# Optimization experiments

Measured on AMD Instinct MI355X. Metric: run time of the kernel, lower is better.

## Reference

```python
import jax, jax.numpy as jnp
import numpy as np

B, H = 8, 8
C_IN, C_OUT = 128, 128
E, O = C_IN // H, C_OUT // H              # per-head channels
S = (32, 32, 64)                           # spatial dims (space_dims_q == space_dims_kv)
M = (8, 8, 8)                              # lowest-mode block kept per rfft dim
N_MODES = M[0] * M[1] * M[2]               # 512 = mask.sum()
SCALE = 1.0 / (C_IN * C_OUT)


def setup_inputs() -> dict:
    key = jax.random.key(0)
    k1, k2, k3, k4 = jax.random.split(key, 4)
    q = jax.random.normal(k1, (B, H, E) + S, dtype=jnp.float32)
    k = jax.random.normal(k2, (B, H, E) + S, dtype=jnp.float32)
    # torch.rand(..., dtype=cfloat): real and imag parts each uniform [0,1), scaled
    w_re = jax.random.uniform(k3, (H, E, O, N_MODES), dtype=jnp.float32) * SCALE
    w_im = jax.random.uniform(k4, (H, E, O, N_MODES), dtype=jnp.float32) * SCALE
    return {"q": q, "k": k, "w_re": w_re, "w_im": w_im}


def _select_modes(x_ft):
    # block low-mode mask -> slice + flatten (C order, matches torch bool indexing)
    m0, m1, m2 = M
    return x_ft[..., :m0, :m1, :m2].reshape(x_ft.shape[:3] + (-1,))


def reference(q, k, w_re, w_im):
    m0, m1, m2 = M
    xq_ft = jnp.fft.rfftn(q, axes=(3, 4, 5), norm='ortho')   # [B,H,E,32,32,33] c64
    xk_ft = jnp.fft.rfftn(k, axes=(3, 4, 5), norm='ortho')
    xq_sel = _select_modes(xq_ft)                             # [B,H,E,Mq]
    xk_sel = _select_modes(xk_ft)                             # [B,H,E,Mkv]
    w = jax.lax.complex(w_re, w_im)                           # [H,E,O,Mq]

    # complex attention: no conjugation, complex tanh (matches torch)
    att = jnp.tanh(jnp.einsum('bhex,bhey->bhxy', xq_sel, xk_sel))
    xqkv = jnp.einsum('bhxy,bhey->bhex', att, xk_sel)         # [B,H,E,Mq]
    xqkvw = jnp.einsum('bhex,heox->bhox', xqkv, w)            # [B,H,O,Mq]

    out_ft = jnp.zeros((q.shape[0], H, O, S[0], S[1], S[2] // 2 + 1),
                       dtype=xqkvw.dtype)
    out_ft = out_ft.at[..., :m0, :m1, :m2].set(
        xqkvw.reshape(q.shape[0], H, O, m0, m1, m2))

    # canonical_fft_freq over dims (3,4): x <- (x + conj(x[-i mod s0, -j mod s1]))/2
    neg = jnp.roll(jnp.flip(out_ft, axis=(3, 4)), shift=(1, 1), axis=(3, 4))
    out_ft = (out_ft + jnp.conj(neg)) * 0.5

    out = jnp.fft.irfftn(out_ft / (C_IN * C_OUT), axes=(3, 4, 5), s=S, norm='ortho')
    return out  # original returns (out, None)
```

## Files before the change

### kernel.cpp

```cpp
#include <hip/hip_runtime.h>

#define PI_F 3.14159265358979323846f

template<int v> struct ic_t { static constexpr int value = v; };

template<int N, int I = 0, typename F>
__device__ __forceinline__ void sfor(F&& f) {
  if constexpr (I < N) { f(ic_t<I>{}); sfor<N, I + 1>(static_cast<F&&>(f)); }
}

__host__ __device__ constexpr int fold_idx(int t) {
  t &= 63;
  return (t <= 16) ? t : (t <= 32) ? (32 - t) : (t <= 48) ? (t - 32) : (64 - t);
}
__host__ __device__ constexpr float fold_sgn(int t) {
  t &= 63;
  return (t <= 16) ? 1.f : (t <= 48) ? -1.f : 1.f;
}

__device__ constexpr float CCV[17] = {
  1.0f, 0.9951847266721969f, 0.9807852804032304f, 0.9569403357322088f,
  0.9238795325112867f, 0.8819212643483550f, 0.8314696123025452f,
  0.7730104533627370f, 0.7071067811865476f, 0.6343932841636455f,
  0.5555702330196022f, 0.4713967368259976f, 0.3826834323650898f,
  0.2902846772544623f, 0.1950903220161283f, 0.0980171403295606f, 0.0f};

#define TCOS(T) (fold_sgn(T) * CCV[fold_idx(T)])
#define TSIN(T) (fold_sgn(((T) + 48) & 63) * CCV[fold_idx(((T) + 48) & 63)])

template<int G>
__device__ __forceinline__ void row_group(const float4& qa, const float4& qb,
                                          const float4& qc, const float4& qd,
                                          float* Xr, float* Xi)
{
  sfor<4>([&](auto MC) {
    constexpr int m = decltype(MC)::value;
    constexpr int j = 4 * G + m;
    const float xa = (m == 0) ? qa.x : (m == 1) ? qa.y : (m == 2) ? qa.z : qa.w;
    const float xb = (m == 0) ? qb.x : (m == 1) ? qb.y : (m == 2) ? qb.z : qb.w;
    const float xc = (m == 0) ? qc.x : (m == 1) ? qc.y : (m == 2) ? qc.z : qc.w;
    const float xd = (m == 0) ? qd.x : (m == 1) ? qd.y : (m == 2) ? qd.z : qd.w;
    const float s02 = xa + xc, d02 = xa - xc;
    const float s13 = xb + xd, d31 = xd - xb;
    const float g0 = s02 + s13, g2 = s02 - s13;
    Xr[0] += g0;
    sfor<3>([&](auto EC) {
      constexpr int k2 = 2 * (decltype(EC)::value + 1);
      constexpr int t = (k2 * j) & 63;
      const float g = (k2 == 4) ? g0 : g2;
      Xr[k2] = fmaf(g,  TCOS(t), Xr[k2]);
      Xi[k2] = fmaf(-g, TSIN(t), Xi[k2]);
    });
    sfor<4>([&](auto UC) {
      constexpr int k2 = 2 * decltype(UC)::value + 1;
      constexpr int t = (k2 * j) & 63;
      const float gr = d02;
      const float gi = ((k2 & 3) == 1) ? d31 : -d31;
      Xr[k2] = fmaf(gr, TCOS(t), fmaf(gi,  TSIN(t), Xr[k2]));
      Xi[k2] = fmaf(gi, TCOS(t), fmaf(-gr, TSIN(t), Xi[k2]));
    });
  });
}

__global__ __launch_bounds__(512, 4)
void k1_fwd_dft(const float* __restrict__ qg, const float* __restrict__ kg,
                float2* __restrict__ qsel, float2* __restrict__ ksel)
{
  __shared__ float2 Yb[8 * 1036];
  __shared__ float2 tw32[32];

  const int tid = threadIdx.x;
  const int lane = tid & 63;
  const int wv = tid >> 6;
  const int bid = blockIdx.x;
  const int ch = bid & 1023;
  const float* __restrict__ src = (bid < 1024 ? qg : kg) + (size_t)ch * 65536;
  float2* __restrict__ dst = (bid < 1024 ? qsel : ksel) + ch * 512;

  if (tid < 32) {
    float s, c;
    sincosf((float)tid * (2.f * PI_F / 32.f), &s, &c);
    tw32[tid] = make_float2(c, s);
  }

  #pragma unroll
  for (int p = 0; p < 2; ++p) {
    const int row = (p << 9) + tid;
    const float4* __restrict__ rq = (const float4*)(src + ((size_t)row << 6));
    float Xr[8], Xi[8];
    sfor<8>([&](auto K) { constexpr int k = decltype(K)::value;
      Xr[k] = 0.f; Xi[k] = 0.f; });

    float4 A0 = rq[0], A1 = rq[4], A2 = rq[8],  A3 = rq[12];
    float4 B0 = rq[1], B1 = rq[5], B2 = rq[9],  B3 = rq[13];
    __builtin_amdgcn_sched_barrier(0);
    row_group<0>(A0, A1, A2, A3, Xr, Xi);
    __builtin_amdgcn_sched_barrier(0);
    A0 = rq[2]; A1 = rq[6]; A2 = rq[10]; A3 = rq[14];
    __builtin_amdgcn_sched_barrier(0);
    row_group<1>(B0, B1, B2, B3, Xr, Xi);
    __builtin_amdgcn_sched_barrier(0);
    B0 = rq[3]; B1 = rq[7]; B2 = rq[11]; B3 = rq[15];
    __builtin_amdgcn_sched_barrier(0);
    row_group<2>(A0, A1, A2, A3, Xr, Xi);
    __builtin_amdgcn_sched_barrier(0);
    row_group<3>(B0, B1, B2, B3, Xr, Xi);

    sfor<8>([&](auto KC) {
      constexpr int k2 = decltype(KC)::value;
      Yb[k2 * 1036 + row] = make_float2(Xr[k2], Xi[k2]);
    });
  }
  __syncthreads();

  const int k1 = lane >> 3;
  const int k2 = lane & 7;
  float Wr[8], Wi[8];
  sfor<8>([&](auto K) { constexpr int k = decltype(K)::value;
    Wr[k] = 0.f; Wi[k] = 0.f; });

  sfor<4>([&](auto QC) {
    constexpr int q = decltype(QC)::value;
    const int n0 = wv + 8 * q;
    const float2* __restrict__ yp = &Yb[k2 * 1036 + n0 * 32];
    float zr = 0.f, zi = 0.f;
    #pragma unroll
    for (int n1 = 0; n1 < 32; ++n1) {
      const float2 y = yp[n1];
      const float2 w = tw32[(k1 * n1) & 31];
      zr = fmaf(y.x, w.x, fmaf( y.y, w.y, zr));
      zi = fmaf(y.y, w.x, fmaf(-y.x, w.y, zi));
    }
    sfor<8>([&](auto KC) {
      constexpr int k0 = decltype(KC)::value;
      const float2 w = tw32[(k0 * n0) & 31];
      Wr[k0] = fmaf(zr, w.x, fmaf( zi, w.y, Wr[k0]));
      Wi[k0] = fmaf(zi, w.x, fmaf(-zr, w.y, Wi[k0]));
    });
  });
  __syncthreads();

  float2* __restrict__ part = Yb;
  sfor<8>([&](auto KC) {
    constexpr int k0 = decltype(KC)::value;
    part[k0 * 512 + (wv << 6) + lane] = make_float2(Wr[k0], Wi[k0]);
  });
  __syncthreads();

  {
    const float2* __restrict__ pp = &part[(wv << 9) + lane];
    float sr = 0.f, si = 0.f;
    #pragma unroll
    for (int w8 = 0; w8 < 8; ++w8) {
      const float2 v = pp[w8 * 64];
      sr += v.x; si += v.y;
    }
    dst[tid] = make_float2(sr * (1.f / 256.f), si * (1.f / 256.f));
  }
}

__global__ __launch_bounds__(512, 4)
void k2_attn(const float2* __restrict__ qsel, const float2* __restrict__ ksel,
             float2* __restrict__ xqkv)
{
  __shared__ float2 Kl[8192];
  const int tid = threadIdx.x;
  const int bh = blockIdx.x >> 3;
  const int xo = blockIdx.x & 7;

  const float2* __restrict__ kb = ksel + bh * 8192;
  for (int i = tid; i < 8192; i += 512) Kl[i] = kb[i];

  const int xr = tid & 63;
  const int yh = tid >> 6;
  const int x = xo * 64 + xr;
  const float2* __restrict__ qb = qsel + bh * 8192;
  float qr[16], qi[16], ar[16], ai[16];
  sfor<16>([&](auto E) {
    constexpr int e = decltype(E)::value;
    const float2 v = qb[e * 512 + x];
    qr[e] = v.x; qi[e] = v.y;
    ar[e] = 0.f; ai[e] = 0.f;
  });
  __syncthreads();

  const int y0 = yh * 64;
  for (int y = y0; y < y0 + 64; ++y) {
    float kr[16], ki[16];
    float sr = 0.f, si = 0.f;
    sfor<16>([&](auto E) {
      constexpr int e = decltype(E)::value;
      const float2 v = Kl[e * 512 + y];
      kr[e] = v.x; ki[e] = v.y;
      sr = fmaf(qr[e], v.x, fmaf(-qi[e], v.y, sr));
      si = fmaf(qr[e], v.y, fmaf( qi[e], v.x, si));
    });
    float a2 = 2.f * sr;
    a2 = fminf(fmaxf(a2, -30.f), 30.f);
    const float b2 = 2.f * si;
    const float ea = expf(a2);
    const float ei = 1.f / ea;
    const float sh = 0.5f * (ea - ei);
    const float chp = 0.5f * (ea + ei);
    float sb, cb;
    sincosf(b2, &sb, &cb);
    const float inv = 1.f / (chp + cb);
    const float tr = sh * inv;
    const float ti = sb * inv;
    sfor<16>([&](auto E) {
      constexpr int e = decltype(E)::value;
      ar[e] = fmaf(tr, kr[e], fmaf(-ti, ki[e], ar[e]));
      ai[e] = fmaf(tr, ki[e], fmaf( ti, kr[e], ai[e]));
    });
  }
  __syncthreads();
  float* __restrict__ red = (float*)Kl;
  if (yh) {
    const int g = yh - 1;
    sfor<16>([&](auto E) {
      constexpr int e = decltype(E)::value;
      red[(g * 32 + 2 * e) * 64 + xr] = ar[e];
      red[(g * 32 + 2 * e + 1) * 64 + xr] = ai[e];
    });
  }
  __syncthreads();
  if (!yh) {
    float2* __restrict__ ob = xqkv + bh * 8192;
    sfor<16>([&](auto E) {
      constexpr int e = decltype(E)::value;
      float sr2 = ar[e], si2 = ai[e];
      #pragma unroll
      for (int g = 0; g < 7; ++g) {
        sr2 += red[(g * 32 + 2 * e) * 64 + xr];
        si2 += red[(g * 32 + 2 * e + 1) * 64 + xr];
      }
      ob[e * 512 + x] = make_float2(sr2, si2);
    });
  }
}

#define SCALE_OUT (1.f / 4194304.f)

__global__ __launch_bounds__(256, 2)
void k3_inv(const float2* __restrict__ xqkv, const float* __restrict__ w_re,
            const float* __restrict__ w_im, float* __restrict__ out)
{
  __shared__ float2 Fs[512];
  __shared__ float cn[64];
  __shared__ float Ur[4096], Ui[4096];
  __shared__ float Vr[2048], Vi[2048];

  const int tid = threadIdx.x;
  const int bho = blockIdx.x;
  const int o = bho & 15;
  const int h = (bho >> 4) & 7;
  const int bh = bho >> 4;

  if (tid < 64) cn[tid] = cosf((float)tid * (PI_F / 32.f));

  float cc[17];
  sfor<17>([&](auto J) { constexpr int j = decltype(J)::value;
    cc[j] = cosf((float)j * (PI_F / 32.f)); });
  #define TCOSr(T) (fold_sgn(T) * cc[fold_idx(T)])
  #define TSINr(T) (fold_sgn(((T) + 48) & 63) * cc[fold_idx(((T) + 48) & 63)])

  const float2* __restrict__ xb = xqkv + bh * 8192;
  const float* __restrict__ wrb = w_re + ((size_t)(h * 256 + o)) * 512;
  const float* __restrict__ wib = w_im + ((size_t)(h * 256 + o)) * 512;
  for (int x = tid; x < 512; x += 256) {
    float fr = 0.f, fi = 0.f;
    sfor<16>([&](auto E) {
      constexpr int e = decltype(E)::value;
      const float2 v = xb[e * 512 + x];
      const float wr = wrb[e * 8192 + x];
      const float wi = wib[e * 8192 + x];
      fr = fmaf(v.x, wr, fmaf(-v.y, wi, fr));
      fi = fmaf(v.x, wi, fmaf( v.y, wr, fi));
    });
    Fs[x] = make_float2(fr * SCALE_OUT, fi * SCALE_OUT);
  }
  __syncthreads();

  const int n2 = tid & 63;
  const int wv = tid >> 6;

  #pragma unroll
  for (int i = 0; i < 16; ++i) {
    const int p = wv * 16 + i;
    float ur = 0.f, ui = 0.f;
    sfor<8>([&](auto KC) {
      constexpr int k2 = decltype(KC)::value;
      const float2 f = Fs[p * 8 + k2];
      const float cv = cn[(k2 * n2) & 63];
      const float wgt = (k2 == 0) ? cv : 2.f * cv;
      ur = fmaf(wgt, f.x, ur);
      ui = fmaf(wgt, f.y, ui);
    });
    Ur[p * 64 + n2] = ur;
    Ui[p * 64 + n2] = ui;
  }
  __syncthreads();

  float u_r[2][8], u_i[2][8];
  sfor<2>([&](auto JC) {
    constexpr int j = decltype(JC)::value;
    sfor<8>([&](auto KC) {
      constexpr int k1 = decltype(KC)::value;
      const int p = (wv * 2 + j) * 8 + k1;
      u_r[j][k1] = Ur[p * 64 + n2];
      u_i[j][k1] = Ui[p * 64 + n2];
    });
  });

  float* __restrict__ ob = out + (size_t)bho * 65536;

  for (int chq = 0; chq < 8; ++chq) {
    sfor<2>([&](auto JC) {
      constexpr int j = decltype(JC)::value;
      const int k0 = wv * 2 + j;
      sfor<4>([&](auto LC) {
        constexpr int l = decltype(LC)::value;
        const int n1 = chq * 4 + l;
        float vr = 0.f, vi = 0.f;
        sfor<8>([&](auto KC) {
          constexpr int k1 = decltype(KC)::value;
          const int t = (2 * k1 * n1) & 63;
          const float cv = cn[t];
          const float sv = cn[(t + 48) & 63];
          vr = fmaf(u_r[j][k1], cv, fmaf(-u_i[j][k1], sv, vr));
          vi = fmaf(u_r[j][k1], sv, fmaf( u_i[j][k1], cv, vi));
        });
        Vr[(k0 * 4 + l) * 64 + n2] = vr;
        Vi[(k0 * 4 + l) * 64 + n2] = vi;
      });
    });
    __syncthreads();
    {
      const int l = wv;
      float vrr[8], vii[8];
      sfor<8>([&](auto KC) {
        constexpr int k0 = decltype(KC)::value;
        vrr[k0] = Vr[(k0 * 4 + l) * 64 + n2];
        vii[k0] = Vi[(k0 * 4 + l) * 64 + n2];
      });
      const int n1 = chq * 4 + l;
      float* __restrict__ op = ob + n1 * 64 + n2;
      sfor<32>([&](auto NC) {
        constexpr int n0 = decltype(NC)::value;
        float acc = vrr[0];
        sfor<7>([&](auto KC) {
          constexpr int k0 = decltype(KC)::value + 1;
          constexpr int t = (2 * k0 * n0) & 63;
          acc = fmaf(vrr[k0], TCOSr(t), fmaf(-vii[k0], TSINr(t), acc));
        });
        op[n0 * 2048] = acc;
      });
    }
    __syncthreads();
  }
}

extern "C" void kernel_launch(void* const* d_in, const int* in_sizes, int n_in,
                              void* d_out, int out_size, void* d_ws, size_t ws_size,
                              hipStream_t stream)
{
  (void)in_sizes; (void)n_in; (void)out_size; (void)ws_size;
  const float* q    = (const float*)d_in[0];
  const float* k    = (const float*)d_in[1];
  const float* w_re = (const float*)d_in[2];
  const float* w_im = (const float*)d_in[3];
  float* out = (float*)d_out;

  float2* qsel = (float2*)d_ws;
  float2* ksel = qsel + 1024 * 512;
  float2* xqkv = ksel + 1024 * 512;

  hipLaunchKernelGGL(k1_fwd_dft, dim3(2048), dim3(512), 0, stream, q, k, qsel, ksel);
  hipLaunchKernelGGL(k2_attn,    dim3(512),  dim3(512), 0, stream, qsel, ksel, xqkv);
  hipLaunchKernelGGL(k3_inv,     dim3(1024), dim3(256), 0, stream, xqkv, w_re, w_im, out);
}
```

Before: 307.4 us.

## Split attention E-reduction across half-waves and use fast exp/sincos intrinsics

The attention kernel now splits the 16 per-head channels across the two halves of each wavefront, with 8 channels per lane, and combines the partial dot products using a cross-lane shuffle. The grid doubles to 1024 blocks, each covering 32 query modes. This is meant to cut per-thread register pressure and raise parallelism in the tanh-attention loop, which was likely limited by occupancy and latency. It also switches to the __expf/__sincosf fast intrinsics, which costs some accuracy, and each block must still load the full K tile into LDS, so global-to-LDS K traffic doubles.

```diff
diff --git a/kernel.cpp b/kernel.cpp
--- a/kernel.cpp
+++ b/kernel.cpp
@@ -165,76 +165,82 @@
 {
   __shared__ float2 Kl[8192];
   const int tid = threadIdx.x;
-  const int bh = blockIdx.x >> 3;
-  const int xo = blockIdx.x & 7;
+  const int bh = blockIdx.x >> 4;
+  const int xo = blockIdx.x & 15;
 
   const float2* __restrict__ kb = ksel + bh * 8192;
   for (int i = tid; i < 8192; i += 512) Kl[i] = kb[i];
 
-  const int xr = tid & 63;
-  const int yh = tid >> 6;
-  const int x = xo * 64 + xr;
+  const int lane = tid & 63;
+  const int yg = tid >> 6;
+  const int xl = lane & 31;
+  const int eh = lane >> 5;
+  const int x = xo * 32 + xl;
+  const int e0 = eh * 8;
+
   const float2* __restrict__ qb = qsel + bh * 8192;
-  float qr[16], qi[16], ar[16], ai[16];
-  sfor<16>([&](auto E) {
-    constexpr int e = decltype(E)::value;
-    const float2 v = qb[e * 512 + x];
-    qr[e] = v.x; qi[e] = v.y;
-    ar[e] = 0.f; ai[e] = 0.f;
-  });
-  __syncthreads();
-
-  const int y0 = yh * 64;
+  float qr[8], qi[8], ar[8], ai[8];
+  sfor<8>([&](auto E) {
+    constexpr int el = decltype(E)::value;
+    const float2 v = qb[(e0 + el) * 512 + x];
+    qr[el] = v.x; qi[el] = v.y;
+    ar[el] = 0.f; ai[el] = 0.f;
+  });
+  __syncthreads();
+
+  const int y0 = yg * 64;
   for (int y = y0; y < y0 + 64; ++y) {
-    float kr[16], ki[16];
+    float kr[8], ki[8];
     float sr = 0.f, si = 0.f;
-    sfor<16>([&](auto E) {
-      constexpr int e = decltype(E)::value;
-      const float2 v = Kl[e * 512 + y];
-      kr[e] = v.x; ki[e] = v.y;
-      sr = fmaf(qr[e], v.x, fmaf(-qi[e], v.y, sr));
-      si = fmaf(qr[e], v.y, fmaf( qi[e], v.x, si));
-    });
+    sfor<8>([&](auto E) {
+      constexpr int el = decltype(E)::value;
+      const float2 v = Kl[(e0 + el) * 512 + y];
+      kr[el] = v.x; ki[el] = v.y;
+      sr = fmaf(qr[el], v.x, fmaf(-qi[el], v.y, sr));
+      si = fmaf(qr[el], v.y, fmaf( qi[el], v.x, si));
+    });
+    sr += __shfl_xor(sr, 32);
+    si += __shfl_xor(si, 32);
     float a2 = 2.f * sr;
     a2 = fminf(fmaxf(a2, -30.f), 30.f);
     const float b2 = 2.f * si;
-    const float ea = expf(a2);
+    const float ea = __expf(a2);
     const float ei = 1.f / ea;
     const float sh = 0.5f * (ea - ei);
     const float chp = 0.5f * (ea + ei);
     float sb, cb;
-    sincosf(b2, &sb, &cb);
+    __sincosf(b2, &sb, &cb);
     const float inv = 1.f / (chp + cb);
     const float tr = sh * inv;
     const float ti = sb * inv;
-    sfor<16>([&](auto E) {
-      constexpr int e = decltype(E)::value;
-      ar[e] = fmaf(tr, kr[e], fmaf(-ti, ki[e], ar[e]));
-      ai[e] = fmaf(tr, ki[e], fmaf( ti, kr[e], ai[e]));
+    sfor<8>([&](auto E) {
+      constexpr int el = decltype(E)::value;
+      ar[el] = fmaf(tr, kr[el], fmaf(-ti, ki[el], ar[el]));
+      ai[el] = fmaf(tr, ki[el], fmaf( ti, kr[el], ai[el]));
     });
   }
   __syncthreads();
   float* __restrict__ red = (float*)Kl;
-  if (yh) {
-    const int g = yh - 1;
-    sfor<16>([&](auto E) {
-      constexpr int e = decltype(E)::value;
-      red[(g * 32 + 2 * e) * 64 + xr] = ar[e];
-      red[(g * 32 + 2 * e + 1) * 64 + xr] = ai[e];
-    });
-  }
-  __syncthreads();
-  if (!yh) {
+  if (yg) {
+    const int g = yg - 1;
+    sfor<8>([&](auto E) {
+      constexpr int el = decltype(E)::value;
+      red[g * 1024 + (eh * 8 + el) * 64 + 2 * xl]     = ar[el];
+      red[g * 1024 + (eh * 8 + el) * 64 + 2 * xl + 1] = ai[el];
+    });
+  }
+  __syncthreads();
+  if (!yg) {
     float2* __restrict__ ob = xqkv + bh * 8192;
-    sfor<16>([&](auto E) {
-      constexpr int e = decltype(E)::value;
-      float sr2 = ar[e], si2 = ai[e];
+    sfor<8>([&](auto E) {
+      constexpr int el = decltype(E)::value;
+      float sr2 = ar[el], si2 = ai[el];
       #pragma unroll
       for (int g = 0; g < 7; ++g) {
-        sr2 += red[(g * 32 + 2 * e) * 64 + xr];
-        si2 += red[(g * 32 + 2 * e + 1) * 64 + xr];
+        sr2 += red[g * 1024 + (eh * 8 + el) * 64 + 2 * xl];
+        si2 += red[g * 1024 + (eh * 8 + el) * 64 + 2 * xl + 1];
       }
-      ob[e * 512 + x] = make_float2(sr2, si2);
+      ob[(e0 + el) * 512 + x] = make_float2(sr2, si2);
     });
   }
 }
@@ -376,6 +382,6 @@
   float2* xqkv = ksel + 1024 * 512;
 
   hipLaunchKernelGGL(k1_fwd_dft, dim3(2048), dim3(512), 0, stream, q, k, qsel, ksel);
-  hipLaunchKernelGGL(k2_attn,    dim3(512),  dim3(512), 0, stream, qsel, ksel, xqkv);
+  hipLaunchKernelGGL(k2_attn,    dim3(1024), dim3(512), 0, stream, qsel, ksel, xqkv);
   hipLaunchKernelGGL(k3_inv,     dim3(1024), dim3(256), 0, stream, xqkv, w_re, w_im, out);
 }
```

Measured after the change: 311.5 us. No clear change (+1.3%).
